# Performance work log

Measured on AMD Instinct MI355X. Metric: run time of the kernel, lower is better.

The kernel has to match this reference:

```python
import jax, jax.numpy as jnp
import numpy as np

N = 8192
IN_DIM = 256
OUT_DIM = 128
ALPHA = 0.2  # LeakyReLU negative slope
MASK_VAL = -9e15


def setup_inputs() -> dict:
    key = jax.random.key(0)
    k1, k2, k3, k4 = jax.random.split(key, 4)
    adjacency = jax.random.randint(k1, (N, N), 0, 2, dtype=jnp.int32)
    X = jax.random.normal(k2, (N, IN_DIM), dtype=jnp.float32)
    # kaiming-normal-ish scale
    W = jax.random.normal(k3, (IN_DIM, OUT_DIM), dtype=jnp.float32) * np.sqrt(2.0 / IN_DIM)
    a = jax.random.normal(k4, (2 * OUT_DIM, 1), dtype=jnp.float32) * np.sqrt(2.0 / (2 * OUT_DIM))
    return {"adjacency": adjacency, "X": X, "W": W, "a": a}


def reference(adjacency, X, W, a):
    Wh = X @ W  # [N, D]
    # e[i,j] = lrelu([Wh_i ; Wh_j] @ a) = lrelu(Wh@a1 + (Wh@a2)^T)
    a1 = a[:OUT_DIM, 0]   # [D]
    a2 = a[OUT_DIM:, 0]   # [D]
    e = (Wh @ a1)[:, None] + (Wh @ a2)[None, :]  # [N, N]
    e = jax.nn.leaky_relu(e, negative_slope=ALPHA)
    scores = jnp.where(adjacency > 0, e, jnp.asarray(MASK_VAL, e.dtype))
    attention = jax.nn.softmax(scores, axis=1)  # dropout p=0 -> identity
    h_prime = attention @ Wh  # [N, D]
    return jax.nn.elu(h_prime)
```

## Files before the change

### kernel.cpp

```cpp
#include <hip/hip_runtime.h>
#include <hip/hip_bf16.h>

#define NN 8192
#define KDIM 256
#define DDIM 128

typedef __attribute__((ext_vector_type(8))) short short8;
typedef __attribute__((ext_vector_type(4))) float floatx4;
typedef __attribute__((ext_vector_type(4))) int intx4;

__device__ __forceinline__ unsigned short f2bf(float x) {
    unsigned int u = __float_as_uint(x);
    return (unsigned short)((u + 0x8000u) >> 16);
}

__global__ void k_trip(float* out, float v) {
    if (threadIdx.x == 0 && blockIdx.x == 0) out[0] = v;
}

__global__ void kA_swizzleW(const float* __restrict__ W, unsigned short* __restrict__ WB) {
    int gid = blockIdx.x * blockDim.x + threadIdx.x;
    int kt = gid >> 9, nt = (gid >> 6) & 7, lane = gid & 63;
    int quad = lane >> 4, c = lane & 15;
    short8 pack;
#pragma unroll
    for (int t = 0; t < 8; ++t)
        pack[t] = (short)f2bf(W[(kt * 32 + quad * 8 + t) * DDIM + nt * 16 + c]);
    *(short8*)(WB + ((size_t)(kt * 8 + nt) * 64 + lane) * 8) = pack;
}

__global__ __launch_bounds__(256) void kB_wh(
        const float* __restrict__ X,
        const unsigned short* __restrict__ WB,
        const float* __restrict__ a,
        unsigned short* __restrict__ WhB,
        float* __restrict__ f, float* __restrict__ g) {
    __shared__ unsigned short tile[64 * 128];
    int tid = threadIdx.x;
    int wave = tid >> 6, lane = tid & 63;
    int quad = lane >> 4, c = lane & 15;
    int rowbase = blockIdx.x * 64 + wave * 16;

    floatx4 acc[8];
#pragma unroll
    for (int nt = 0; nt < 8; ++nt) acc[nt] = (floatx4)(0.0f);

    const short8* WB8 = (const short8*)WB;
#pragma unroll
    for (int ks = 0; ks < 8; ++ks) {
        const float* xp = X + (size_t)(rowbase + c) * KDIM + ks * 32 + quad * 8;
        floatx4 x0 = *(const floatx4*)xp;
        floatx4 x1 = *(const floatx4*)(xp + 4);
        short8 afrag;
#pragma unroll
        for (int t = 0; t < 4; ++t) { afrag[t] = (short)f2bf(x0[t]); afrag[4 + t] = (short)f2bf(x1[t]); }
#pragma unroll
        for (int nt = 0; nt < 8; ++nt) {
            short8 b = WB8[(ks * 8 + nt) * 64 + lane];
            acc[nt] = __builtin_amdgcn_mfma_f32_16x16x32_bf16(afrag, b, acc[nt], 0, 0, 0);
        }
    }

    float fp[4] = {0.f, 0.f, 0.f, 0.f}, gp[4] = {0.f, 0.f, 0.f, 0.f};
#pragma unroll
    for (int nt = 0; nt < 8; ++nt) {
        float a1 = a[nt * 16 + c];
        float a2 = a[DDIM + nt * 16 + c];
#pragma unroll
        for (int r = 0; r < 4; ++r) {
            fp[r] += acc[nt][r] * a1;
            gp[r] += acc[nt][r] * a2;
        }
    }
#pragma unroll
    for (int m = 1; m < 16; m <<= 1) {
#pragma unroll
        for (int r = 0; r < 4; ++r) {
            fp[r] += __shfl_xor(fp[r], m);
            gp[r] += __shfl_xor(gp[r], m);
        }
    }
    if (c == 0) {
#pragma unroll
        for (int r = 0; r < 4; ++r) {
            f[rowbase + quad * 4 + r] = fp[r];
            g[rowbase + quad * 4 + r] = gp[r];
        }
    }

#pragma unroll
    for (int nt = 0; nt < 8; ++nt)
#pragma unroll
        for (int r = 0; r < 4; ++r)
            tile[(wave * 16 + quad * 4 + r) * 128 + nt * 16 + c] = f2bf(acc[nt][r]);
    __syncthreads();

    int kt2 = wave >> 1;
#pragma unroll
    for (int ntj = 0; ntj < 4; ++ntj) {
        int nt = (wave & 1) * 4 + ntj;
        short8 pack;
#pragma unroll
        for (int t = 0; t < 8; ++t)
            pack[t] = (short)tile[(kt2 * 32 + quad * 8 + t) * 128 + nt * 16 + c];
        *(short8*)(WhB + ((size_t)((blockIdx.x * 2 + kt2) * 8 + nt) * 64 + lane) * 8) = pack;
    }
}

__global__ __launch_bounds__(256, 4) void kC_attn(
        const int* __restrict__ adj,
        const unsigned short* __restrict__ WhB,
        const float* __restrict__ f, const float* __restrict__ g,
        float* __restrict__ pacc, float* __restrict__ pl) {
    __shared__ float smem[8192];
    int tid = threadIdx.x;
    int wave = tid >> 6, lane = tid & 63;
    int quad = lane >> 4, c = lane & 15;
    int bq   = blockIdx.x >> 9;
    int brow = blockIdx.x & 511;
    int rowbase = brow * 16;

    {
        const floatx4* g4 = (const floatx4*)g;
        for (int i = tid; i < 1024; i += 256)
            ((floatx4*)smem)[i] = g4[bq * 1024 + i];
    }
    __syncthreads();

    float f0 = f[rowbase + c];

    floatx4 acc[8];
#pragma unroll
    for (int nt = 0; nt < 8; ++nt) acc[nt] = (floatx4)(0.0f);
    float l0 = 0.0f;

    const intx4* arow = (const intx4*)(adj + (size_t)(rowbase + c) * NN);
    const short8* WhB8 = (const short8*)WhB;
    int jbase = bq * 128;

    intx4 A0a = arow[(jbase + 0 * 4 + wave) * 8 + quad * 2];
    intx4 A0b = arow[(jbase + 0 * 4 + wave) * 8 + quad * 2 + 1];
    intx4 A1a = arow[(jbase + 1 * 4 + wave) * 8 + quad * 2];
    intx4 A1b = arow[(jbase + 1 * 4 + wave) * 8 + quad * 2 + 1];

    short8 bfrA[8], bfrB[8];
#pragma unroll
    for (int nt = 0; nt < 8; ++nt)
        bfrA[nt] = WhB8[((size_t)(jbase + wave) * 8 + nt) * 64 + lane];

#define KC_STEP(ITC, BCUR, BNEXT) do {                                          \
        int j4n_ = jbase + (((ITC) + 2) & 31) * 4 + wave;                       \
        intx4 A2a_ = arow[j4n_ * 8 + quad * 2];                                 \
        intx4 A2b_ = arow[j4n_ * 8 + quad * 2 + 1];                             \
        int J32n_ = jbase + (((ITC) + 1) & 31) * 4 + wave;                      \
        _Pragma("unroll")                                                       \
        for (int nt = 0; nt < 8; ++nt)                                          \
            BNEXT[nt] = WhB8[((size_t)J32n_ * 8 + nt) * 64 + lane];             \
        int gb_ = ((ITC) * 4 + wave) * 32 + quad * 8;                           \
        floatx4 g0_ = *(const floatx4*)&smem[gb_];                              \
        floatx4 g1_ = *(const floatx4*)&smem[gb_ + 4];                          \
        short8 afr_;                                                            \
        _Pragma("unroll")                                                       \
        for (int u = 0; u < 4; ++u) {                                           \
            float x_, E_;                                                       \
            x_ = f0 + g0_[u]; x_ = fmaxf(x_, 0.2f * x_);                        \
            E_ = (A0a[u] > 0) ? __expf(x_) : 0.0f; l0 += E_;                    \
            afr_[u] = (short)f2bf(E_);                                          \
            x_ = f0 + g1_[u]; x_ = fmaxf(x_, 0.2f * x_);                        \
            E_ = (A0b[u] > 0) ? __expf(x_) : 0.0f; l0 += E_;                    \
            afr_[4 + u] = (short)f2bf(E_);                                      \
        }                                                                       \
        _Pragma("unroll")                                                       \
        for (int nt = 0; nt < 8; ++nt)                                          \
            acc[nt] = __builtin_amdgcn_mfma_f32_16x16x32_bf16(afr_, BCUR[nt],   \
                                                              acc[nt], 0, 0, 0);\
        A0a = A1a; A0b = A1b; A1a = A2a_; A1b = A2b_;                           \
    } while (0)

    for (int it = 0; it < 32; it += 2) {
        KC_STEP(it, bfrA, bfrB);
        KC_STEP(it + 1, bfrB, bfrA);
    }
#undef KC_STEP

    __syncthreads();
    smem[7000 + wave * 64 + lane] = l0;
    __syncthreads();
    if (tid < 16) {
        float s = 0.0f;
#pragma unroll
        for (int w = 0; w < 4; ++w)
#pragma unroll
            for (int q = 0; q < 4; ++q)
                s += smem[7000 + w * 64 + q * 16 + tid];
        pl[bq * NN + rowbase + tid] = s;
    }

    if (wave >= 2) {
        float* b = &smem[(wave - 2) * 2304 + lane * 36];
#pragma unroll
        for (int nt = 0; nt < 8; ++nt) *(floatx4*)&b[nt * 4] = acc[nt];
    }
    __syncthreads();
    if (wave < 2) {
        float* b = &smem[wave * 2304 + lane * 36];
#pragma unroll
        for (int nt = 0; nt < 8; ++nt) acc[nt] += *(const floatx4*)&b[nt * 4];
    }
    __syncthreads();
    if (wave == 1) {
        float* b = &smem[lane * 36];
#pragma unroll
        for (int nt = 0; nt < 8; ++nt) *(floatx4*)&b[nt * 4] = acc[nt];
    }
    __syncthreads();

    if (wave == 0) {
        float* b = &smem[lane * 36];
#pragma unroll
        for (int nt = 0; nt < 8; ++nt) acc[nt] += *(const floatx4*)&b[nt * 4];
        float* pb = pacc + (size_t)bq * NN * DDIM;
#pragma unroll
        for (int nt = 0; nt < 8; ++nt)
#pragma unroll
            for (int r = 0; r < 4; ++r)
                pb[(size_t)(rowbase + quad * 4 + r) * DDIM + nt * 16 + c] = acc[nt][r];
    }
}

__global__ __launch_bounds__(256) void kD_merge(
        const float* __restrict__ pacc, const float* __restrict__ pl,
        float* __restrict__ out) {
    int i = blockIdx.x * 256 + threadIdx.x;
    const floatx4* p4 = (const floatx4*)pacc;
    floatx4 a = p4[i];
    floatx4 b = p4[i + NN * DDIM / 4];
    int row = i >> 5;
    float s = pl[row] + pl[NN + row];
    float inv = (s > 0.0f) ? 1.0f / s : 0.0f;
    floatx4 h;
#pragma unroll
    for (int r = 0; r < 4; ++r) {
        float v = (a[r] + b[r]) * inv;
        h[r] = (v > 0.0f) ? v : expm1f(v);
    }
    ((floatx4*)out)[i] = h;
}

extern "C" void kernel_launch(void* const* d_in, const int* in_sizes, int n_in,
                              void* d_out, int out_size, void* d_ws, size_t ws_size,
                              hipStream_t stream) {
    float* out = (float*)d_out;

    const void *p_adj = nullptr, *p_X = nullptr, *p_W = nullptr, *p_a = nullptr;
    for (int i = 0; i < n_in; ++i) {
        switch (in_sizes[i]) {
            case NN * NN:     p_adj = d_in[i]; break;
            case NN * KDIM:   p_X   = d_in[i]; break;
            case KDIM * DDIM: p_W   = d_in[i]; break;
            case 2 * DDIM:    p_a   = d_in[i]; break;
            default: break;
        }
    }
    if (!p_adj || !p_X || !p_W || !p_a) {
        k_trip<<<dim3(1), dim3(64), 0, stream>>>(out, 99999.0f);
        return;
    }

    size_t off_WB   = 0;
    size_t off_WhB  = off_WB + 65536;
    size_t off_f    = off_WhB + (size_t)NN * DDIM * 2;
    size_t off_g    = off_f + NN * 4;
    size_t off_pacc = off_g + NN * 4;
    size_t off_pl   = off_pacc + (size_t)2 * NN * DDIM * 4;
    size_t needed   = off_pl + (size_t)2 * NN * 4;
    if (ws_size < needed) {
        k_trip<<<dim3(1), dim3(64), 0, stream>>>(out, 12345.0f);
        return;
    }
    char* ws = (char*)d_ws;
    unsigned short* WB   = (unsigned short*)(ws + off_WB);
    unsigned short* WhB  = (unsigned short*)(ws + off_WhB);
    float*          f    = (float*)(ws + off_f);
    float*          g    = (float*)(ws + off_g);
    float*          pacc = (float*)(ws + off_pacc);
    float*          pl   = (float*)(ws + off_pl);

    const int*   adj = (const int*)p_adj;
    const float* X   = (const float*)p_X;
    const float* W   = (const float*)p_W;
    const float* a   = (const float*)p_a;

    kA_swizzleW<<<dim3(16), dim3(256), 0, stream>>>(W, WB);
    kB_wh<<<dim3(128), dim3(256), 0, stream>>>(X, WB, a, WhB, f, g);
    kC_attn<<<dim3(1024), dim3(256), 0, stream>>>(adj, WhB, f, g, pacc, pl);
    kD_merge<<<dim3(NN * DDIM / 4 / 256), dim3(256), 0, stream>>>(pacc, pl, out);
}
```

Baseline: 430.9 us.

## Split attention key dimension four ways with higher-occupancy kernel and four-way merge

```diff
diff --git a/kernel.cpp b/kernel.cpp
--- a/kernel.cpp
+++ b/kernel.cpp
@@ -107,7 +107,147 @@
     }
 }
 
-__global__ __launch_bounds__(256, 4) void kC_attn(
+__global__ __launch_bounds__(256, 8) void kC_attn4(
+        const int* __restrict__ adj,
+        const unsigned short* __restrict__ WhB,
+        const float* __restrict__ f, const float* __restrict__ g,
+        float* __restrict__ pacc, float* __restrict__ pl) {
+    __shared__ float smem[4880];
+    int tid = threadIdx.x;
+    int wave = tid >> 6, lane = tid & 63;
+    int quad = lane >> 4, c = lane & 15;
+    int bq   = blockIdx.x >> 9;
+    int brow = blockIdx.x & 511;
+    int rowbase = brow * 16;
+
+    {
+        const floatx4* g4 = (const floatx4*)g;
+        for (int i = tid; i < 512; i += 256)
+            ((floatx4*)smem)[i] = g4[bq * 512 + i];
+    }
+    __syncthreads();
+
+    float f0 = f[rowbase + c];
+
+    floatx4 acc[8];
+#pragma unroll
+    for (int nt = 0; nt < 8; ++nt) acc[nt] = (floatx4)(0.0f);
+    float l0 = 0.0f;
+
+    const intx4* arow = (const intx4*)(adj + (size_t)(rowbase + c) * NN);
+    const short8* WhB8 = (const short8*)WhB;
+    int jbase = bq * 64;
+
+    intx4 A0a = arow[(jbase + 0 * 4 + wave) * 8 + quad * 2];
+    intx4 A0b = arow[(jbase + 0 * 4 + wave) * 8 + quad * 2 + 1];
+    intx4 A1a = arow[(jbase + 1 * 4 + wave) * 8 + quad * 2];
+    intx4 A1b = arow[(jbase + 1 * 4 + wave) * 8 + quad * 2 + 1];
+
+    short8 bfrA[8], bfrB[8];
+#pragma unroll
+    for (int nt = 0; nt < 8; ++nt)
+        bfrA[nt] = WhB8[((size_t)(jbase + wave) * 8 + nt) * 64 + lane];
+
+#define KC_STEP(ITC, BCUR, BNEXT) do {                                          \
+        int j4n_ = jbase + (((ITC) + 2) & 15) * 4 + wave;                       \
+        intx4 A2a_ = arow[j4n_ * 8 + quad * 2];                                 \
+        intx4 A2b_ = arow[j4n_ * 8 + quad * 2 + 1];                             \
+        int J32n_ = jbase + (((ITC) + 1) & 15) * 4 + wave;                      \
+        _Pragma("unroll")                                                       \
+        for (int nt = 0; nt < 8; ++nt)                                          \
+            BNEXT[nt] = WhB8[((size_t)J32n_ * 8 + nt) * 64 + lane];             \
+        int gb_ = ((ITC) * 4 + wave) * 32 + quad * 8;                           \
+        floatx4 g0_ = *(const floatx4*)&smem[gb_];                              \
+        floatx4 g1_ = *(const floatx4*)&smem[gb_ + 4];                          \
+        short8 afr_;                                                            \
+        _Pragma("unroll")                                                       \
+        for (int u = 0; u < 4; ++u) {                                           \
+            float x_, E_;                                                       \
+            x_ = f0 + g0_[u]; x_ = fmaxf(x_, 0.2f * x_);                        \
+            E_ = (A0a[u] > 0) ? __expf(x_) : 0.0f; l0 += E_;                    \
+            afr_[u] = (short)f2bf(E_);                                          \
+            x_ = f0 + g1_[u]; x_ = fmaxf(x_, 0.2f * x_);                        \
+            E_ = (A0b[u] > 0) ? __expf(x_) : 0.0f; l0 += E_;                    \
+            afr_[4 + u] = (short)f2bf(E_);                                      \
+        }                                                                       \
+        _Pragma("unroll")                                                       \
+        for (int nt = 0; nt < 8; ++nt)                                          \
+            acc[nt] = __builtin_amdgcn_mfma_f32_16x16x32_bf16(afr_, BCUR[nt],   \
+                                                              acc[nt], 0, 0, 0);\
+        A0a = A1a; A0b = A1b; A1a = A2a_; A1b = A2b_;                           \
+    } while (0)
+
+    for (int it = 0; it < 16; it += 2) {
+        KC_STEP(it, bfrA, bfrB);
+        KC_STEP(it + 1, bfrB, bfrA);
+    }
+#undef KC_STEP
+
+    __syncthreads();
+    smem[4608 + wave * 64 + lane] = l0;
+    __syncthreads();
+    if (tid < 16) {
+        float s = 0.0f;
+#pragma unroll
+        for (int w = 0; w < 4; ++w)
+#pragma unroll
+            for (int q = 0; q < 4; ++q)
+                s += smem[4608 + w * 64 + q * 16 + tid];
+        pl[bq * NN + rowbase + tid] = s;
+    }
+
+    if (wave >= 2) {
+        float* b = &smem[(wave - 2) * 2304 + lane * 36];
+#pragma unroll
+        for (int nt = 0; nt < 8; ++nt) *(floatx4*)&b[nt * 4] = acc[nt];
+    }
+    __syncthreads();
+    if (wave < 2) {
+        float* b = &smem[wave * 2304 + lane * 36];
+#pragma unroll
+        for (int nt = 0; nt < 8; ++nt) acc[nt] += *(const floatx4*)&b[nt * 4];
+    }
+    __syncthreads();
+    if (wave == 1) {
+        float* b = &smem[lane * 36];
+#pragma unroll
+        for (int nt = 0; nt < 8; ++nt) *(floatx4*)&b[nt * 4] = acc[nt];
+    }
+    __syncthreads();
+
+    if (wave == 0) {
+        float* b = &smem[lane * 36];
+#pragma unroll
+        for (int nt = 0; nt < 8; ++nt) acc[nt] += *(const floatx4*)&b[nt * 4];
+        float* pb = pacc + (size_t)bq * NN * DDIM;
+#pragma unroll
+        for (int nt = 0; nt < 8; ++nt)
+#pragma unroll
+            for (int r = 0; r < 4; ++r)
+                pb[(size_t)(rowbase + quad * 4 + r) * DDIM + nt * 16 + c] = acc[nt][r];
+    }
+}
+
+__global__ __launch_bounds__(256) void kD_merge4(
+        const float* __restrict__ pacc, const float* __restrict__ pl,
+        float* __restrict__ out) {
+    int i = blockIdx.x * 256 + threadIdx.x;
+    const int Q = NN * DDIM / 4;
+    const floatx4* p4 = (const floatx4*)pacc;
+    floatx4 a0 = p4[i], a1 = p4[i + Q], a2 = p4[i + 2 * Q], a3 = p4[i + 3 * Q];
+    int row = i >> 5;
+    float s = pl[row] + pl[NN + row] + pl[2 * NN + row] + pl[3 * NN + row];
+    float inv = (s > 0.0f) ? 1.0f / s : 0.0f;
+    floatx4 h;
+#pragma unroll
+    for (int r = 0; r < 4; ++r) {
+        float v = (a0[r] + a1[r] + a2[r] + a3[r]) * inv;
+        h[r] = (v > 0.0f) ? v : expm1f(v);
+    }
+    ((floatx4*)out)[i] = h;
+}
+
+__global__ __launch_bounds__(256, 4) void kC_attn2(
         const int* __restrict__ adj,
         const unsigned short* __restrict__ WhB,
         const float* __restrict__ f, const float* __restrict__ g,
@@ -228,7 +368,7 @@
     }
 }
 
-__global__ __launch_bounds__(256) void kD_merge(
+__global__ __launch_bounds__(256) void kD_merge2(
         const float* __restrict__ pacc, const float* __restrict__ pl,
         float* __restrict__ out) {
     int i = blockIdx.x * 256 + threadIdx.x;
@@ -272,9 +412,9 @@
     size_t off_f    = off_WhB + (size_t)NN * DDIM * 2;
     size_t off_g    = off_f + NN * 4;
     size_t off_pacc = off_g + NN * 4;
-    size_t off_pl   = off_pacc + (size_t)2 * NN * DDIM * 4;
-    size_t needed   = off_pl + (size_t)2 * NN * 4;
-    if (ws_size < needed) {
+    size_t needed4  = off_pacc + (size_t)4 * NN * DDIM * 4 + (size_t)4 * NN * 4;
+    size_t needed2  = off_pacc + (size_t)2 * NN * DDIM * 4 + (size_t)2 * NN * 4;
+    if (ws_size < needed2) {
         k_trip<<<dim3(1), dim3(64), 0, stream>>>(out, 12345.0f);
         return;
     }
@@ -284,7 +424,6 @@
     float*          f    = (float*)(ws + off_f);
     float*          g    = (float*)(ws + off_g);
     float*          pacc = (float*)(ws + off_pacc);
-    float*          pl   = (float*)(ws + off_pl);
 
     const int*   adj = (const int*)p_adj;
     const float* X   = (const float*)p_X;
@@ -293,6 +432,14 @@
 
     kA_swizzleW<<<dim3(16), dim3(256), 0, stream>>>(W, WB);
     kB_wh<<<dim3(128), dim3(256), 0, stream>>>(X, WB, a, WhB, f, g);
-    kC_attn<<<dim3(1024), dim3(256), 0, stream>>>(adj, WhB, f, g, pacc, pl);
-    kD_merge<<<dim3(NN * DDIM / 4 / 256), dim3(256), 0, stream>>>(pacc, pl, out);
-}
+
+    if (ws_size >= needed4) {
+        float* pl = (float*)(ws + off_pacc + (size_t)4 * NN * DDIM * 4);
+        kC_attn4<<<dim3(2048), dim3(256), 0, stream>>>(adj, WhB, f, g, pacc, pl);
+        kD_merge4<<<dim3(NN * DDIM / 4 / 256), dim3(256), 0, stream>>>(pacc, pl, out);
+    } else {
+        float* pl = (float*)(ws + off_pacc + (size_t)2 * NN * DDIM * 4);
+        kC_attn2<<<dim3(1024), dim3(256), 0, stream>>>(adj, WhB, f, g, pacc, pl);
+        kD_merge2<<<dim3(NN * DDIM / 4 / 256), dim3(256), 0, stream>>>(pacc, pl, out);
+    }
+}
```

New measurement: 675.4 us. 56.7% more time.
